# Kernel tuning notes

Hardware: AMD Instinct MI355X
Metric: run time of the kernel (lower is better)

The kernel has to match this reference:

```python
import jax, jax.numpy as jnp
import numpy as np

ALPHA = 0.1
BETA = 1.1
NUM_CLASSES = 16
EPS = 1e-8  # matches torch cosine_similarity eps
BATCH = 131072
DIM = 512


def setup_inputs() -> dict:
    key = jax.random.key(0)
    k1, k2 = jax.random.split(key)
    embeddings = jax.random.normal(k1, (BATCH, DIM), dtype=jnp.float32)
    labels = jax.random.randint(k2, (BATCH,), 0, NUM_CLASSES)
    return {"embeddings": embeddings, "labels": labels}


def _cos_dist(a, b):
    # a: [M, D], b: [N, D] -> 1 - cosine_similarity, shape [M, N]
    an = a / jnp.maximum(jnp.linalg.norm(a, axis=-1, keepdims=True), EPS)
    bn = b / jnp.maximum(jnp.linalg.norm(b, axis=-1, keepdims=True), EPS)
    return 1.0 - an @ bn.T


def reference(embeddings, labels):
    C = NUM_CLASSES
    N = embeddings.shape[0]
    dt = embeddings.dtype

    # class centroids (dummy anchors) via scatter-mean
    cnt = jax.ops.segment_sum(jnp.ones((N,), dt), labels, num_segments=C)  # [C]
    sums = jax.ops.segment_sum(embeddings, labels, num_segments=C)        # [C, D]
    centroids = sums / jnp.maximum(cnt, 1.0)[:, None]
    present = cnt > 0

    # close class pairs: i < j, both present, centroid distance <= beta
    pd = _cos_dist(centroids, centroids)                    # [C, C]
    upper = jnp.triu(jnp.ones((C, C), bool), k=1)
    pairmask = upper & (pd <= BETA) & present[:, None] & present[None, :]
    pm = pairmask.astype(dt)
    deg = pm.sum(1) + pm.sum(0)                             # pairs involving each class

    # distances from every centroid to every sample
    D = _cos_dist(centroids, embeddings)                    # [C, N]

    # intra: each sample of class c contributes relu(d(cent_c, x) - alpha),
    # once per close pair involving c
    d_own = D[labels, jnp.arange(N)]                        # [N]
    intra_sum = jnp.sum(deg[labels] * jax.nn.relu(d_own - ALPHA))

    # inter: S[c, c'] = sum over samples with label c' of relu(beta - d(cent_c, x))
    S = jax.ops.segment_sum(jax.nn.relu(BETA - D).T, labels, num_segments=C).T  # [C, C]
    inter_sum = jnp.sum(pm * (S + S.T))

    # number of terms in each loss list: sum over pairs of (cnt_i + cnt_j)
    count = jnp.sum(deg * cnt)
    denom = jnp.maximum(count, 1.0)
    num_pairs = pm.sum()

    loss = jnp.where(num_pairs > 0, intra_sum / denom + inter_sum / denom, 0.0)
    return loss
```

## Files before the change

### kernel.cpp

```cpp
#include <hip/hip_runtime.h>

constexpr float kAlpha = 0.1f;
constexpr float kBeta  = 1.1f;
constexpr int   kC     = 16;
constexpr int   kD     = 512;
constexpr float kEps   = 1e-8f;

constexpr int SUMS_OFF = 0;
constexpr int CNT_OFF  = 8192;
constexpr int TOT_OFF  = 8208;
constexpr int CN_OFF   = 8224;
constexpr int MSK_OFF  = 16416;
constexpr int SCL_OFF  = 16432;
constexpr int ZERO_FLOATS = 8209;

__global__ __launch_bounds__(256) void k1_sums(const float* __restrict__ emb,
                                               const int* __restrict__ labels,
                                               float* __restrict__ sums,
                                               float* __restrict__ cnt,
                                               int N, int rows_per_block) {
    __shared__ float2 lsum2[kC * kD / 2];
    __shared__ float  lcnt[kC];
    int tid = threadIdx.x;
    float* lf = (float*)lsum2;
    for (int i = tid; i < kC * kD; i += 256) lf[i] = 0.f;
    if (tid < kC) lcnt[tid] = 0.f;
    __syncthreads();

    int r0 = blockIdx.x * rows_per_block;
    int r1 = min(r0 + rows_per_block, N);
    const float2* e2 = (const float2*)emb;
    for (int r = r0; r < r1; ++r) {
        int l = labels[r];
        float2 v = e2[(size_t)r * (kD / 2) + tid];
        float2* p = &lsum2[l * (kD / 2) + tid];
        p->x += v.x;
        p->y += v.y;
        if (tid == 0) lcnt[l] += 1.f;
    }
    __syncthreads();
    for (int i = tid; i < kC * kD; i += 256) atomicAdd(&sums[i], lf[i]);
    if (tid < kC) atomicAdd(&cnt[tid], lcnt[tid]);
}

__global__ __launch_bounds__(256) void k2_cent(const float* __restrict__ sums,
                                               const float* __restrict__ cnt_g,
                                               float* __restrict__ cn_g,
                                               unsigned* __restrict__ mask_g,
                                               float* __restrict__ scal) {
    __shared__ __align__(16) float lcn[kC * kD];
    __shared__ float lcnt[kC];
    __shared__ float red[256];
    __shared__ float norms[kC];
    __shared__ float pdm[kC * kC];
    int tid = threadIdx.x;
    if (tid < kC) lcnt[tid] = cnt_g[tid];
    __syncthreads();

    int c = tid >> 4, sub = tid & 15;
    float invc = 1.f / fmaxf(lcnt[c], 1.f);
    float sq = 0.f;
    for (int d = sub; d < kD; d += 16) {
        float v = sums[c * kD + d] * invc;
        lcn[c * kD + d] = v;
        sq += v * v;
    }
    red[tid] = sq;
    __syncthreads();
    if (tid < kC) {
        float t = 0.f;
        for (int k = 0; k < 16; ++k) t += red[tid * 16 + k];
        norms[tid] = fmaxf(sqrtf(t), kEps);
    }
    __syncthreads();
    for (int i = tid; i < kC * kD; i += 256) {
        float v = lcn[i] / norms[i / kD];
        lcn[i] = v;
        cn_g[i] = v;
    }
    __syncthreads();
    int pi = tid >> 4, pj = tid & 15;
    float dot = 0.f;
    for (int dd = 0; dd < kD; ++dd) {
        int d = (dd + tid) & (kD - 1);
        dot += lcn[pi * kD + d] * lcn[pj * kD + d];
    }
    pdm[tid] = 1.f - dot;
    __syncthreads();
    if (tid == 0) {
        unsigned m[kC];
        for (int a = 0; a < kC; ++a) m[a] = 0u;
        float npairs = 0.f;
        for (int a = 0; a < kC; ++a)
            for (int b = a + 1; b < kC; ++b) {
                bool close = (pdm[a * kC + b] <= kBeta) && (lcnt[a] > 0.f) && (lcnt[b] > 0.f);
                if (close) { m[a] |= 1u << b; m[b] |= 1u << a; npairs += 1.f; }
            }
        float count = 0.f;
        for (int a = 0; a < kC; ++a) {
            mask_g[a] = m[a];
            count += (float)__popc(m[a]) * lcnt[a];
        }
        scal[0] = fmaxf(count, 1.f);
        scal[1] = npairs;
    }
}

__global__ __launch_bounds__(256) void k3_main(const float* __restrict__ emb,
                                               const int* __restrict__ labels,
                                               const float* __restrict__ cn_g,
                                               const unsigned* __restrict__ mask_g,
                                               float* __restrict__ total,
                                               int N, int half) {
    __shared__ __align__(16) float lcn[kC * kD];
    __shared__ unsigned lmask[kC];
    __shared__ float wsum[4];
    int tid = threadIdx.x;
    for (int i = tid; i < kC * kD; i += 256) lcn[i] = cn_g[i];
    if (tid < kC) lmask[tid] = mask_g[tid];
    __syncthreads();

    int r0 = blockIdx.x * 256 + tid;
    int r1 = r0 + half;
    bool v0 = (r0 < half) && (r0 < N);
    bool v1 = v0 && (r1 < N);

    float dots0[kC], dots1[kC];
#pragma unroll
    for (int cc = 0; cc < kC; ++cc) { dots0[cc] = 0.f; dots1[cc] = 0.f; }
    float n0 = 0.f, n1 = 0.f;

    int rr0 = v0 ? r0 : 0;
    int rr1 = v1 ? r1 : 0;
    const float4* row0 = (const float4*)(emb + (size_t)rr0 * kD);
    const float4* row1 = (const float4*)(emb + (size_t)rr1 * kD);
    const float4* w4 = (const float4*)lcn;

    for (int it = 0; it < kD / 4; ++it) {
        float4 x0 = row0[it];
        float4 x1 = row1[it];
        n0 += x0.x * x0.x + x0.y * x0.y + x0.z * x0.z + x0.w * x0.w;
        n1 += x1.x * x1.x + x1.y * x1.y + x1.z * x1.z + x1.w * x1.w;
#pragma unroll
        for (int cc = 0; cc < kC; ++cc) {
            float4 w = w4[cc * (kD / 4) + it];
            dots0[cc] += x0.x * w.x + x0.y * w.y + x0.z * w.z + x0.w * w.w;
            dots1[cc] += x1.x * w.x + x1.y * w.y + x1.z * w.z + x1.w * w.w;
        }
    }

    float contrib = 0.f;
    {
        int l = v0 ? labels[rr0] : 0;
        unsigned m = lmask[l];
        float inv = 1.f / fmaxf(sqrtf(n0), kEps);
        float down = 0.f;
#pragma unroll
        for (int cc = 0; cc < kC; ++cc) down = (cc == l) ? (1.f - dots0[cc] * inv) : down;
        float s = (float)__popc(m) * fmaxf(down - kAlpha, 0.f);
#pragma unroll
        for (int cc = 0; cc < kC; ++cc) {
            float dd = 1.f - dots0[cc] * inv;
            s += ((m >> cc) & 1u) ? fmaxf(kBeta - dd, 0.f) : 0.f;
        }
        contrib += v0 ? s : 0.f;
    }
    {
        int l = v1 ? labels[rr1] : 0;
        unsigned m = lmask[l];
        float inv = 1.f / fmaxf(sqrtf(n1), kEps);
        float down = 0.f;
#pragma unroll
        for (int cc = 0; cc < kC; ++cc) down = (cc == l) ? (1.f - dots1[cc] * inv) : down;
        float s = (float)__popc(m) * fmaxf(down - kAlpha, 0.f);
#pragma unroll
        for (int cc = 0; cc < kC; ++cc) {
            float dd = 1.f - dots1[cc] * inv;
            s += ((m >> cc) & 1u) ? fmaxf(kBeta - dd, 0.f) : 0.f;
        }
        contrib += v1 ? s : 0.f;
    }

#pragma unroll
    for (int off = 32; off > 0; off >>= 1) contrib += __shfl_down(contrib, off, 64);
    if ((tid & 63) == 0) wsum[tid >> 6] = contrib;
    __syncthreads();
    if (tid == 0) atomicAdd(total, wsum[0] + wsum[1] + wsum[2] + wsum[3]);
}

__global__ void k4_final(const float* __restrict__ total,
                         const float* __restrict__ scal,
                         float* __restrict__ out) {
    out[0] = (scal[1] > 0.f) ? (total[0] / scal[0]) : 0.f;
}

extern "C" void kernel_launch(void* const* d_in, const int* in_sizes, int n_in,
                              void* d_out, int out_size, void* d_ws, size_t ws_size,
                              hipStream_t stream) {
    const float* emb = (const float*)d_in[0];
    const int* labels = (const int*)d_in[1];
    int N = in_sizes[0] / kD;

    float* ws = (float*)d_ws;
    float* sums = ws + SUMS_OFF;
    float* cnt = ws + CNT_OFF;
    float* total = ws + TOT_OFF;
    float* cn = ws + CN_OFF;
    unsigned* mask = (unsigned*)(ws + MSK_OFF);
    float* scal = ws + SCL_OFF;

    hipMemsetAsync(d_ws, 0, ZERO_FLOATS * sizeof(float), stream);

    int blocks1 = 512;
    int rpb = (N + blocks1 - 1) / blocks1;
    k1_sums<<<blocks1, 256, 0, stream>>>(emb, labels, sums, cnt, N, rpb);

    k2_cent<<<1, 256, 0, stream>>>(sums, cnt, cn, mask, scal);

    int half = (N + 1) >> 1;
    int blocks3 = (half + 255) / 256;
    k3_main<<<blocks3, 256, 0, stream>>>(emb, labels, cn, mask, total, N, half);

    k4_final<<<1, 1, 0, stream>>>(total, scal, (float*)d_out);
}
```

Before: 613.2 us.

## Coalesce row loads in sums and distance kernels via register accumulators and lane-split dots

```diff
diff --git a/kernel.cpp b/kernel.cpp
--- a/kernel.cpp
+++ b/kernel.cpp
@@ -14,33 +14,57 @@
 constexpr int SCL_OFF  = 16432;
 constexpr int ZERO_FLOATS = 8209;
 
-__global__ __launch_bounds__(256) void k1_sums(const float* __restrict__ emb,
+__global__ __launch_bounds__(512) void k1_sums(const float* __restrict__ emb,
                                                const int* __restrict__ labels,
                                                float* __restrict__ sums,
                                                float* __restrict__ cnt,
-                                               int N, int rows_per_block) {
-    __shared__ float2 lsum2[kC * kD / 2];
-    __shared__ float  lcnt[kC];
+                                               int N, int rpb) {
     int tid = threadIdx.x;
-    float* lf = (float*)lsum2;
-    for (int i = tid; i < kC * kD; i += 256) lf[i] = 0.f;
-    if (tid < kC) lcnt[tid] = 0.f;
-    __syncthreads();
-
-    int r0 = blockIdx.x * rows_per_block;
-    int r1 = min(r0 + rows_per_block, N);
-    const float2* e2 = (const float2*)emb;
-    for (int r = r0; r < r1; ++r) {
+    int myc = tid & 15;
+    float acc[kC];
+#pragma unroll
+    for (int c = 0; c < kC; ++c) acc[c] = 0.f;
+    float cacc = 0.f;
+
+    int r0 = blockIdx.x * rpb;
+    int r1 = min(r0 + rpb, N);
+    int r = r0;
+    for (; r + 8 <= r1; r += 8) {
+        int4 la = *(const int4*)(labels + r);
+        int4 lb = *(const int4*)(labels + r + 4);
+        const float* e = emb + (size_t)r * kD + tid;
+        float v0 = e[0 * kD];
+        float v1 = e[1 * kD];
+        float v2 = e[2 * kD];
+        float v3 = e[3 * kD];
+        float v4 = e[4 * kD];
+        float v5 = e[5 * kD];
+        float v6 = e[6 * kD];
+        float v7 = e[7 * kD];
+#pragma unroll
+        for (int c = 0; c < kC; ++c) {
+            float s = (la.x == c ? v0 : 0.f) + (la.y == c ? v1 : 0.f)
+                    + (la.z == c ? v2 : 0.f) + (la.w == c ? v3 : 0.f)
+                    + (lb.x == c ? v4 : 0.f) + (lb.y == c ? v5 : 0.f)
+                    + (lb.z == c ? v6 : 0.f) + (lb.w == c ? v7 : 0.f);
+            acc[c] += s;
+        }
+        cacc += (la.x == myc ? 1.f : 0.f) + (la.y == myc ? 1.f : 0.f)
+              + (la.z == myc ? 1.f : 0.f) + (la.w == myc ? 1.f : 0.f)
+              + (lb.x == myc ? 1.f : 0.f) + (lb.y == myc ? 1.f : 0.f)
+              + (lb.z == myc ? 1.f : 0.f) + (lb.w == myc ? 1.f : 0.f);
+    }
+    for (; r < r1; ++r) {
         int l = labels[r];
-        float2 v = e2[(size_t)r * (kD / 2) + tid];
-        float2* p = &lsum2[l * (kD / 2) + tid];
-        p->x += v.x;
-        p->y += v.y;
-        if (tid == 0) lcnt[l] += 1.f;
-    }
-    __syncthreads();
-    for (int i = tid; i < kC * kD; i += 256) atomicAdd(&sums[i], lf[i]);
-    if (tid < kC) atomicAdd(&cnt[tid], lcnt[tid]);
+        float v = emb[(size_t)r * kD + tid];
+#pragma unroll
+        for (int c = 0; c < kC; ++c) acc[c] += (l == c ? v : 0.f);
+        cacc += (l == myc ? 1.f : 0.f);
+    }
+
+#pragma unroll
+    for (int c = 0; c < kC; ++c) atomicAdd(&sums[c * kD + tid], acc[c]);
+    if (tid < kC) atomicAdd(&cnt[tid], cacc);
 }
 
 __global__ __launch_bounds__(256) void k2_cent(const float* __restrict__ sums,
@@ -111,7 +135,7 @@
                                                const float* __restrict__ cn_g,
                                                const unsigned* __restrict__ mask_g,
                                                float* __restrict__ total,
-                                               int N, int half) {
+                                               int N, int rpb) {
     __shared__ __align__(16) float lcn[kC * kD];
     __shared__ unsigned lmask[kC];
     __shared__ float wsum[4];
@@ -120,70 +144,62 @@
     if (tid < kC) lmask[tid] = mask_g[tid];
     __syncthreads();
 
-    int r0 = blockIdx.x * 256 + tid;
-    int r1 = r0 + half;
-    bool v0 = (r0 < half) && (r0 < N);
-    bool v1 = v0 && (r1 < N);
-
-    float dots0[kC], dots1[kC];
-#pragma unroll
-    for (int cc = 0; cc < kC; ++cc) { dots0[cc] = 0.f; dots1[cc] = 0.f; }
-    float n0 = 0.f, n1 = 0.f;
-
-    int rr0 = v0 ? r0 : 0;
-    int rr1 = v1 ? r1 : 0;
-    const float4* row0 = (const float4*)(emb + (size_t)rr0 * kD);
-    const float4* row1 = (const float4*)(emb + (size_t)rr1 * kD);
+    const int j = tid & 15;
+    const int grp = tid >> 4;
     const float4* w4 = (const float4*)lcn;
 
-    for (int it = 0; it < kD / 4; ++it) {
-        float4 x0 = row0[it];
-        float4 x1 = row1[it];
-        n0 += x0.x * x0.x + x0.y * x0.y + x0.z * x0.z + x0.w * x0.w;
-        n1 += x1.x * x1.x + x1.y * x1.y + x1.z * x1.z + x1.w * x1.w;
-#pragma unroll
-        for (int cc = 0; cc < kC; ++cc) {
-            float4 w = w4[cc * (kD / 4) + it];
-            dots0[cc] += x0.x * w.x + x0.y * w.y + x0.z * w.z + x0.w * w.w;
-            dots1[cc] += x1.x * w.x + x1.y * w.y + x1.z * w.z + x1.w * w.w;
-        }
-    }
-
-    float contrib = 0.f;
-    {
-        int l = v0 ? labels[rr0] : 0;
-        unsigned m = lmask[l];
-        float inv = 1.f / fmaxf(sqrtf(n0), kEps);
-        float down = 0.f;
-#pragma unroll
-        for (int cc = 0; cc < kC; ++cc) down = (cc == l) ? (1.f - dots0[cc] * inv) : down;
-        float s = (float)__popc(m) * fmaxf(down - kAlpha, 0.f);
-#pragma unroll
-        for (int cc = 0; cc < kC; ++cc) {
-            float dd = 1.f - dots0[cc] * inv;
-            s += ((m >> cc) & 1u) ? fmaxf(kBeta - dd, 0.f) : 0.f;
-        }
-        contrib += v0 ? s : 0.f;
-    }
-    {
-        int l = v1 ? labels[rr1] : 0;
-        unsigned m = lmask[l];
-        float inv = 1.f / fmaxf(sqrtf(n1), kEps);
-        float down = 0.f;
-#pragma unroll
-        for (int cc = 0; cc < kC; ++cc) down = (cc == l) ? (1.f - dots1[cc] * inv) : down;
-        float s = (float)__popc(m) * fmaxf(down - kAlpha, 0.f);
-#pragma unroll
-        for (int cc = 0; cc < kC; ++cc) {
-            float dd = 1.f - dots1[cc] * inv;
-            s += ((m >> cc) & 1u) ? fmaxf(kBeta - dd, 0.f) : 0.f;
-        }
-        contrib += v1 ? s : 0.f;
-    }
-
-#pragma unroll
-    for (int off = 32; off > 0; off >>= 1) contrib += __shfl_down(contrib, off, 64);
-    if ((tid & 63) == 0) wsum[tid >> 6] = contrib;
+    float priv = 0.f;
+    int r0 = blockIdx.x * rpb;
+    int r1 = min(r0 + rpb, N);
+    for (int rb = r0; rb < r1; rb += 16) {
+        int r = rb + grp;
+        bool valid = (r < r1);
+        int rc = valid ? r : r0;
+        int lab = labels[rc];
+        const float4* x4 = (const float4*)(emb + (size_t)rc * kD);
+
+        float dots[kC];
+#pragma unroll
+        for (int c = 0; c < kC; ++c) dots[c] = 0.f;
+        float nrm = 0.f;
+
+#pragma unroll
+        for (int it = 0; it < kD / 64; ++it) {
+            float4 x = x4[it * 16 + j];
+            nrm += x.x * x.x + x.y * x.y + x.z * x.z + x.w * x.w;
+#pragma unroll
+            for (int c = 0; c < kC; ++c) {
+                float4 w = w4[c * (kD / 4) + it * 16 + j];
+                dots[c] += x.x * w.x + x.y * w.y + x.z * w.z + x.w * w.w;
+            }
+        }
+
+#pragma unroll
+        for (int m = 1; m < 16; m <<= 1) {
+#pragma unroll
+            for (int c = 0; c < kC; ++c) dots[c] += __shfl_xor(dots[c], m, 64);
+            nrm += __shfl_xor(nrm, m, 64);
+        }
+
+        if (j == 0 && valid) {
+            unsigned mm = lmask[lab];
+            float inv = 1.f / fmaxf(sqrtf(nrm), kEps);
+            float down = 0.f;
+#pragma unroll
+            for (int c = 0; c < kC; ++c) down = (c == lab) ? (1.f - dots[c] * inv) : down;
+            float s = (float)__popc(mm) * fmaxf(down - kAlpha, 0.f);
+#pragma unroll
+            for (int c = 0; c < kC; ++c) {
+                float dd = 1.f - dots[c] * inv;
+                s += ((mm >> c) & 1u) ? fmaxf(kBeta - dd, 0.f) : 0.f;
+            }
+            priv += s;
+        }
+    }
+
+#pragma unroll
+    for (int off = 32; off > 0; off >>= 1) priv += __shfl_down(priv, off, 64);
+    if ((tid & 63) == 0) wsum[tid >> 6] = priv;
     __syncthreads();
     if (tid == 0) atomicAdd(total, wsum[0] + wsum[1] + wsum[2] + wsum[3]);
 }
@@ -212,14 +228,14 @@
     hipMemsetAsync(d_ws, 0, ZERO_FLOATS * sizeof(float), stream);
 
     int blocks1 = 512;
-    int rpb = (N + blocks1 - 1) / blocks1;
-    k1_sums<<<blocks1, 256, 0, stream>>>(emb, labels, sums, cnt, N, rpb);
+    int rpb1 = (N + blocks1 - 1) / blocks1;
+    k1_sums<<<blocks1, 512, 0, stream>>>(emb, labels, sums, cnt, N, rpb1);
 
     k2_cent<<<1, 256, 0, stream>>>(sums, cnt, cn, mask, scal);
 
-    int half = (N + 1) >> 1;
-    int blocks3 = (half + 255) / 256;
-    k3_main<<<blocks3, 256, 0, stream>>>(emb, labels, cn, mask, total, N, half);
+    int blocks3 = 512;
+    int rpb3 = (N + blocks3 - 1) / blocks3;
+    k3_main<<<blocks3, 256, 0, stream>>>(emb, labels, cn, mask, total, N, rpb3);
 
     k4_final<<<1, 1, 0, stream>>>(total, scal, (float*)d_out);
 }
```

Measured after the change: 686.2 us. 11.9% more time.
